# Kernel optimization log

Measured on AMD Instinct MI355X. Metric: run time of the kernel, lower is better.

Reference implementation:

```python
import jax, jax.numpy as jnp
import numpy as np

B, S, D, N, H = 4, 1024, 768, 12, 64
IGNORE = -100000.0


def setup_inputs() -> dict:
    key = jax.random.key(0)
    ks = jax.random.split(key, 9)
    std = 0.02
    return {
        "normalized_resid_pre": jax.random.normal(ks[0], (B, S, D), dtype=jnp.float32),
        "W_Q": jax.random.normal(ks[1], (N, D, H), dtype=jnp.float32) * std,
        "W_K": jax.random.normal(ks[2], (N, D, H), dtype=jnp.float32) * std,
        "W_V": jax.random.normal(ks[3], (N, D, H), dtype=jnp.float32) * std,
        "W_O": jax.random.normal(ks[4], (N, H, D), dtype=jnp.float32) * std,
        "b_Q": jnp.zeros((N, H), dtype=jnp.float32),
        "b_K": jnp.zeros((N, H), dtype=jnp.float32),
        "b_V": jnp.zeros((N, H), dtype=jnp.float32),
        "b_O": jnp.zeros((D,), dtype=jnp.float32),
    }


def reference(normalized_resid_pre, W_Q, W_K, W_V, W_O, b_Q, b_K, b_V, b_O):
    x = normalized_resid_pre  # [b, s, d]
    d_head = W_Q.shape[-1]
    # per-head projections: [b, n, s, h]
    Q = jnp.einsum("bsd,ndh->bnsh", x, W_Q) + b_Q[None, :, None, :]
    K = jnp.einsum("bsd,ndh->bnsh", x, W_K) + b_K[None, :, None, :]
    V = jnp.einsum("bsd,ndh->bnsh", x, W_V) + b_V[None, :, None, :]
    # scores [b, n, s_q, s_k]
    scores = jnp.einsum("bnqh,bnkh->bnqk", Q, K) / jnp.sqrt(jnp.float32(d_head))
    s = scores.shape[-1]
    # original: tril(scores) + triu(IGNORE, k=1) == where(causal, scores, IGNORE)
    causal = jnp.tril(jnp.ones((s, s), dtype=bool))
    masked = jnp.where(causal[None, None], scores, jnp.float32(IGNORE))
    probs = jax.nn.softmax(masked, axis=-1)
    # z [b, s_q, n, h]
    z = jnp.einsum("bnqk,bnkh->bqnh", probs, V)
    out = jnp.einsum("bqnh,nhd->bqd", z, W_O) + b_O
    return out
```

## Files before the change

### kernel.cpp

```cpp
#include <hip/hip_runtime.h>

typedef __bf16 bf16x8 __attribute__((ext_vector_type(8)));
typedef __bf16 bf16x4 __attribute__((ext_vector_type(4)));
typedef float  f32x4  __attribute__((ext_vector_type(4)));

constexpr int B_ = 4, S_ = 1024, D_ = 768, N_ = 12, H_ = 64;
constexpr int BNSH = B_ * N_ * S_ * H_;
constexpr float SCALE2 = 0.18033688011f;

__device__ __forceinline__ f32x4 mfma16(bf16x8 a, bf16x8 b, f32x4 c) {
    return __builtin_amdgcn_mfma_f32_16x16x32_bf16(a, b, c, 0, 0, 0);
}

__device__ __forceinline__ void gload16(const __bf16* g, __bf16* l) {
    __builtin_amdgcn_global_load_lds(
        (const __attribute__((address_space(1))) unsigned int*)g,
        (__attribute__((address_space(3))) unsigned int*)l, 16, 0, 0);
}

__device__ __forceinline__ void stage128x64(const __bf16* g, int ld, __bf16* lds,
                                            int wid, int lane) {
    #pragma unroll
    for (int i = 0; i < 4; ++i) {
        int cb = (wid * 4 + i) * 64;
        int chunk = cb + lane;
        int r = chunk >> 3, p = chunk & 7;
        int q = p ^ (r & 7);
        gload16(g + (size_t)r * ld + q * 8, lds + cb * 8);
    }
}
__device__ __forceinline__ void stage64x64(const __bf16* g, int ld, __bf16* lds,
                                           int wid, int lane) {
    #pragma unroll
    for (int i = 0; i < 2; ++i) {
        int cb = (wid * 2 + i) * 64;
        int chunk = cb + lane;
        int r = chunk >> 3, p = chunk & 7;
        int q = p ^ (r & 7);
        gload16(g + (size_t)r * ld + q * 8, lds + cb * 8);
    }
}

__global__ __launch_bounds__(256) void prep_kernel(
    const float* __restrict__ x,
    const float* __restrict__ wq, const float* __restrict__ wk,
    const float* __restrict__ wv, const float* __restrict__ wo,
    __bf16* __restrict__ xb, __bf16* __restrict__ wt, __bf16* __restrict__ wot) {
    __shared__ __bf16 T[64][65];
    const int blk = blockIdx.x;
    const int tid = threadIdx.x;
    if (blk < 768) {
        int base = blk * 1024 + tid;
        #pragma unroll
        for (int i = 0; i < 4; ++i) {
            int idx = base + i * 256;
            float4 v = ((const float4*)x)[idx];
            bf16x4 o;
            o[0] = (__bf16)v.x; o[1] = (__bf16)v.y;
            o[2] = (__bf16)v.z; o[3] = (__bf16)v.w;
            ((bf16x4*)xb)[idx] = o;
        }
        return;
    }
    int rr = tid >> 4, c4 = (tid & 15) * 4;
    if (blk < 1200) {
        int t = blk - 768;
        int dt = t % 12, mh = t / 12;
        int mat = mh / 12, n = mh % 12;
        const float* in = (mat == 0 ? wq : mat == 1 ? wk : wv) + (size_t)n * 768 * 64;
        __bf16* outp = wt + (size_t)(mat * 768 + n * 64) * 768;
        int d0 = dt * 64;
        #pragma unroll
        for (int i = 0; i < 4; ++i) {
            int row = rr + 16 * i;
            float4 v = *(const float4*)&in[(size_t)(d0 + row) * 64 + c4];
            T[c4 + 0][row] = (__bf16)v.x;
            T[c4 + 1][row] = (__bf16)v.y;
            T[c4 + 2][row] = (__bf16)v.z;
            T[c4 + 3][row] = (__bf16)v.w;
        }
        __syncthreads();
        #pragma unroll
        for (int i = 0; i < 4; ++i) {
            int hrow = rr + 16 * i;
            bf16x4 o;
            o[0] = T[hrow][c4 + 0]; o[1] = T[hrow][c4 + 1];
            o[2] = T[hrow][c4 + 2]; o[3] = T[hrow][c4 + 3];
            *(bf16x4*)&outp[(size_t)hrow * 768 + d0 + c4] = o;
        }
    } else {
        int t = blk - 1200;
        int r0 = (t % 12) * 64, c0 = (t / 12) * 64;
        #pragma unroll
        for (int i = 0; i < 4; ++i) {
            int row = rr + 16 * i;
            float4 v = *(const float4*)&wo[(size_t)(r0 + row) * 768 + c0 + c4];
            T[c4 + 0][row] = (__bf16)v.x;
            T[c4 + 1][row] = (__bf16)v.y;
            T[c4 + 2][row] = (__bf16)v.z;
            T[c4 + 3][row] = (__bf16)v.w;
        }
        __syncthreads();
        #pragma unroll
        for (int i = 0; i < 4; ++i) {
            int crow = rr + 16 * i;
            bf16x4 o;
            o[0] = T[crow][c4 + 0]; o[1] = T[crow][c4 + 1];
            o[2] = T[crow][c4 + 2]; o[3] = T[crow][c4 + 3];
            *(bf16x4*)&wot[(size_t)(c0 + crow) * 768 + r0 + c4] = o;
        }
    }
}

__global__ __launch_bounds__(256) void qkv_gemm(
    const __bf16* __restrict__ xb, const __bf16* __restrict__ wtg,
    const float* __restrict__ bq, const float* __restrict__ bk,
    const float* __restrict__ bv,
    __bf16* __restrict__ Qb, __bf16* __restrict__ Kb, __bf16* __restrict__ Vtb) {
    __shared__ __bf16 As[2][128 * 64];
    __shared__ __bf16 Bs[2][64 * 64];
    const int m0 = blockIdx.x * 128;
    const int j0 = blockIdx.y * 64;
    const int tid = threadIdx.x, wid = tid >> 6, lane = tid & 63;
    const int quad = lane >> 4, lrow = lane & 15;
    const int l3 = lrow & 7;
    int koff[2];
    #pragma unroll
    for (int ks = 0; ks < 2; ++ks)
        koff[ks] = lrow * 64 + ((ks * 4 + quad) ^ l3) * 8;

    f32x4 zf = {0.f, 0.f, 0.f, 0.f};
    f32x4 acc[2][4];
    #pragma unroll
    for (int i = 0; i < 2; ++i)
        #pragma unroll
        for (int j = 0; j < 4; ++j) acc[i][j] = zf;

    stage128x64(xb + (size_t)m0 * 768, 768, As[0], wid, lane);
    stage64x64(wtg + (size_t)j0 * 768, 768, Bs[0], wid, lane);

    for (int kt = 0; kt < 12; ++kt) {
        const int buf = kt & 1;
        __syncthreads();
        if (kt < 11) {
            stage128x64(xb + (size_t)m0 * 768 + (kt + 1) * 64, 768, As[buf ^ 1], wid, lane);
            stage64x64(wtg + (size_t)j0 * 768 + (kt + 1) * 64, 768, Bs[buf ^ 1], wid, lane);
        }
        #pragma unroll
        for (int ks = 0; ks < 2; ++ks) {
            bf16x8 af[2], bfr[4];
            #pragma unroll
            for (int mi = 0; mi < 2; ++mi)
                af[mi] = *(const bf16x8*)(As[buf] + (wid * 32 + mi * 16) * 64 + koff[ks]);
            #pragma unroll
            for (int ni = 0; ni < 4; ++ni)
                bfr[ni] = *(const bf16x8*)(Bs[buf] + ni * 1024 + koff[ks]);
            #pragma unroll
            for (int mi = 0; mi < 2; ++mi)
                #pragma unroll
                for (int ni = 0; ni < 4; ++ni)
                    acc[mi][ni] = mfma16(af[mi], bfr[ni], acc[mi][ni]);
        }
    }

    const int mat = j0 / 768;
    const int n = (j0 % 768) >> 6;
    const int b = m0 >> 10;
    const int s_base = (m0 & 1023) + wid * 32;
    const float* bias = (mat == 0 ? bq : mat == 1 ? bk : bv) + n * 64;
    const float osc = (mat == 0) ? SCALE2 : 1.0f;
    float bias_v[4];
    #pragma unroll
    for (int ni = 0; ni < 4; ++ni) bias_v[ni] = bias[ni * 16 + lrow];

    if (mat == 2) {
        __bf16* vout = Vtb + (size_t)(b * N_ + n) * 64 * 1024;
        #pragma unroll
        for (int mi = 0; mi < 2; ++mi)
            #pragma unroll
            for (int ni = 0; ni < 4; ++ni) {
                int h = ni * 16 + lrow;
                int s0 = s_base + mi * 16 + quad * 4;
                bf16x4 pv;
                #pragma unroll
                for (int r = 0; r < 4; ++r)
                    pv[r] = (__bf16)(acc[mi][ni][r] + bias_v[ni]);
                *(bf16x4*)(vout + (size_t)h * 1024 + s0) = pv;
            }
    } else {
        __bf16* qk = (mat == 0 ? Qb : Kb) + (size_t)(b * N_ + n) * 1024 * 64;
        #pragma unroll
        for (int mi = 0; mi < 2; ++mi)
            #pragma unroll
            for (int r = 0; r < 4; ++r) {
                int s = s_base + mi * 16 + quad * 4 + r;
                #pragma unroll
                for (int ni = 0; ni < 4; ++ni)
                    qk[(size_t)s * 64 + ni * 16 + lrow] =
                        (__bf16)((acc[mi][ni][r] + bias_v[ni]) * osc);
            }
    }
}

__global__ __launch_bounds__(256) void attn_mfma(
    const __bf16* __restrict__ Qb, const __bf16* __restrict__ Kb,
    const __bf16* __restrict__ Vtb, __bf16* __restrict__ zb) {
    __shared__ __bf16 Ks[2][64 * 64], Vs[2][64 * 64];
    __shared__ __bf16 Pt[4][16 * 64];
    const int bid = blockIdx.x;
    const int qt = 15 - bid / 48;
    const int bn = bid % 48;
    const int b = bn / N_, n = bn % N_;
    const int tid = threadIdx.x, wid = tid >> 6, lane = tid & 63;
    const int quad = lane >> 4, lrow = lane & 15;
    const int l3 = lrow & 7;
    const __bf16* Qg = Qb + (size_t)(b * N_ + n) * S_ * H_;
    const __bf16* Kg = Kb + (size_t)(b * N_ + n) * S_ * H_;
    const __bf16* Vg = Vtb + (size_t)(b * N_ + n) * H_ * S_;
    const int q0 = qt * 64;

    int koff[2];
    #pragma unroll
    for (int ks = 0; ks < 2; ++ks)
        koff[ks] = lrow * 64 + ((ks * 4 + quad) ^ l3) * 8;
    int ptw[4], ptr_[2];
    #pragma unroll
    for (int nt = 0; nt < 4; ++nt) {
        int c16 = nt * 2 + (quad >> 1);
        ptw[nt] = lrow * 64 + (c16 ^ l3) * 8 + (quad & 1) * 4;
    }
    #pragma unroll
    for (int ks = 0; ks < 2; ++ks)
        ptr_[ks] = lrow * 64 + ((ks * 4 + quad) ^ l3) * 8;

    bf16x8 qf[2];
    #pragma unroll
    for (int ks = 0; ks < 2; ++ks)
        qf[ks] = *(const bf16x8*)&Qg[(size_t)(q0 + wid * 16 + lrow) * 64
                                     + ks * 32 + quad * 8];

    stage64x64(Kg, 64, Ks[0], wid, lane);
    stage64x64(Vg, 1024, Vs[0], wid, lane);

    f32x4 zf = {0.f, 0.f, 0.f, 0.f};
    f32x4 o[4];
    #pragma unroll
    for (int i = 0; i < 4; ++i) o[i] = zf;
    float l_r = 0.f;
    __bf16* Pw = Pt[wid];
    const int myq = wid * 16 + lrow;

    auto do_tile = [&](int buf, bool diag) {
        f32x4 sc[4];
        #pragma unroll
        for (int nt = 0; nt < 4; ++nt) sc[nt] = zf;
        __builtin_amdgcn_s_setprio(1);
        #pragma unroll
        for (int ks = 0; ks < 2; ++ks) {
            #pragma unroll
            for (int nt = 0; nt < 4; ++nt) {
                bf16x8 kfr = *(const bf16x8*)(Ks[buf] + nt * 1024 + koff[ks]);
                sc[nt] = mfma16(kfr, qf[ks], sc[nt]);
            }
        }
        __builtin_amdgcn_s_setprio(0);
        if (diag) {
            #pragma unroll
            for (int nt = 0; nt < 4; ++nt)
                #pragma unroll
                for (int r = 0; r < 4; ++r)
                    if ((nt * 16 + quad * 4 + r) > myq) sc[nt][r] = -1e30f;
        }
        float rs = 0.f;
        #pragma unroll
        for (int nt = 0; nt < 4; ++nt)
            #pragma unroll
            for (int r = 0; r < 4; ++r) {
                float p = __builtin_amdgcn_exp2f(sc[nt][r]);
                sc[nt][r] = p;
                rs += p;
            }
        l_r += rs;
        #pragma unroll
        for (int nt = 0; nt < 4; ++nt) {
            bf16x4 pk;
            #pragma unroll
            for (int r = 0; r < 4; ++r) pk[r] = (__bf16)sc[nt][r];
            *(bf16x4*)(Pw + ptw[nt]) = pk;
        }
        __builtin_amdgcn_s_setprio(1);
        #pragma unroll
        for (int ks = 0; ks < 2; ++ks) {
            bf16x8 pf = *(const bf16x8*)(Pw + ptr_[ks]);
            #pragma unroll
            for (int ht = 0; ht < 4; ++ht) {
                bf16x8 vfr = *(const bf16x8*)(Vs[buf] + ht * 1024 + koff[ks]);
                o[ht] = mfma16(vfr, pf, o[ht]);
            }
        }
        __builtin_amdgcn_s_setprio(0);
    };

    for (int kt = 0; kt < qt; ++kt) {
        __syncthreads();
        stage64x64(Kg + (size_t)(kt + 1) * 64 * 64, 64, Ks[(kt + 1) & 1], wid, lane);
        stage64x64(Vg + (kt + 1) * 64, 1024, Vs[(kt + 1) & 1], wid, lane);
        do_tile(kt & 1, false);
    }
    __syncthreads();
    do_tile(qt & 1, true);

    l_r += __shfl_xor(l_r, 16);
    l_r += __shfl_xor(l_r, 32);
    const float linv = 1.0f / l_r;
    __bf16* zout = zb + (size_t)b * S_ * 768 + (size_t)(q0 + myq) * 768 + n * 64;
    #pragma unroll
    for (int ht = 0; ht < 4; ++ht) {
        bf16x4 zo;
        #pragma unroll
        for (int r = 0; r < 4; ++r) zo[r] = (__bf16)(o[ht][r] * linv);
        *(bf16x4*)&zout[ht * 16 + quad * 4] = zo;
    }
}

__global__ __launch_bounds__(256) void out_gemm(
    const __bf16* __restrict__ zb, const __bf16* __restrict__ wot,
    const float* __restrict__ bo, float* __restrict__ out) {
    __shared__ __bf16 As[2][64 * 64];
    __shared__ __bf16 Bs[2][64 * 64];
    const int m0 = blockIdx.x * 64;
    const int j0 = blockIdx.y * 64;
    const int tid = threadIdx.x, wid = tid >> 6, lane = tid & 63;
    const int quad = lane >> 4, lrow = lane & 15;
    const int l3 = lrow & 7;
    int koff[2];
    #pragma unroll
    for (int ks = 0; ks < 2; ++ks)
        koff[ks] = lrow * 64 + ((ks * 4 + quad) ^ l3) * 8;

    f32x4 zf = {0.f, 0.f, 0.f, 0.f};
    f32x4 acc[4];
    #pragma unroll
    for (int j = 0; j < 4; ++j) acc[j] = zf;

    stage64x64(zb + (size_t)m0 * 768, 768, As[0], wid, lane);
    stage64x64(wot + (size_t)j0 * 768, 768, Bs[0], wid, lane);

    for (int kt = 0; kt < 12; ++kt) {
        const int buf = kt & 1;
        __syncthreads();
        if (kt < 11) {
            stage64x64(zb + (size_t)m0 * 768 + (kt + 1) * 64, 768, As[buf ^ 1], wid, lane);
            stage64x64(wot + (size_t)j0 * 768 + (kt + 1) * 64, 768, Bs[buf ^ 1], wid, lane);
        }
        #pragma unroll
        for (int ks = 0; ks < 2; ++ks) {
            bf16x8 af = *(const bf16x8*)(As[buf] + wid * 1024 + koff[ks]);
            #pragma unroll
            for (int ni = 0; ni < 4; ++ni) {
                bf16x8 bfr = *(const bf16x8*)(Bs[buf] + ni * 1024 + koff[ks]);
                acc[ni] = mfma16(af, bfr, acc[ni]);
            }
        }
    }

    float bias_v[4];
    #pragma unroll
    for (int ni = 0; ni < 4; ++ni) bias_v[ni] = bo[j0 + ni * 16 + lrow];
    #pragma unroll
    for (int r = 0; r < 4; ++r) {
        int m = m0 + wid * 16 + quad * 4 + r;
        #pragma unroll
        for (int ni = 0; ni < 4; ++ni)
            out[(size_t)m * 768 + j0 + ni * 16 + lrow] = acc[ni][r] + bias_v[ni];
    }
}

extern "C" void kernel_launch(void* const* d_in, const int* in_sizes, int n_in,
                              void* d_out, int out_size, void* d_ws, size_t ws_size,
                              hipStream_t stream) {
    const float* x  = (const float*)d_in[0];
    const float* wq = (const float*)d_in[1];
    const float* wk = (const float*)d_in[2];
    const float* wv = (const float*)d_in[3];
    const float* wo = (const float*)d_in[4];
    const float* bq = (const float*)d_in[5];
    const float* bk = (const float*)d_in[6];
    const float* bv = (const float*)d_in[7];
    const float* bo = (const float*)d_in[8];
    float* out = (float*)d_out;

    __bf16* p   = (__bf16*)d_ws;
    __bf16* xb  = p;  p += (size_t)4096 * 768;
    __bf16* wt  = p;  p += (size_t)2304 * 768;
    __bf16* wot = p;  p += (size_t)768 * 768;
    __bf16* Qb  = p;  p += (size_t)BNSH;
    __bf16* Kb  = p;  p += (size_t)BNSH;
    __bf16* Vtb = p;  p += (size_t)BNSH;
    __bf16* zb  = p;  p += (size_t)4096 * 768;

    prep_kernel<<<1344, 256, 0, stream>>>(x, wq, wk, wv, wo, xb, wt, wot);
    qkv_gemm<<<dim3(32, 36), 256, 0, stream>>>(xb, wt, bq, bk, bv, Qb, Kb, Vtb);
    attn_mfma<<<768, 256, 0, stream>>>(Qb, Kb, Vtb, zb);
    out_gemm<<<dim3(64, 12), 256, 0, stream>>>(zb, wot, bo, out);
}
```

Baseline: 137.3 us.

## Switch attention to 32x32x16 MFMA with register-resident P via permlane swap

Rewrites the attention kernel to use 32x32x16 bf16 MFMA with two waves of 32 query rows each (128 threads) in place of four waves of 16 rows. The softmax probabilities are packed with v_cvt_pk_bf16_f32 and rearranged into the B-operand layout with v_permlane32_swap, which removes the per-wave LDS round trip for P. The aim is fewer LDS reads and writes per FLOP and larger MFMA tiles. The trade-off is fewer waves per block, higher register pressure from the 16-wide accumulators, and each thread now issuing more staging loads.

Result: slower. 141.2 us (+2.9%).

```diff
diff --git a/kernel.cpp b/kernel.cpp
--- a/kernel.cpp
+++ b/kernel.cpp
@@ -3,6 +3,7 @@
 typedef __bf16 bf16x8 __attribute__((ext_vector_type(8)));
 typedef __bf16 bf16x4 __attribute__((ext_vector_type(4)));
 typedef float  f32x4  __attribute__((ext_vector_type(4)));
+typedef float  f32x16 __attribute__((ext_vector_type(16)));
 
 constexpr int B_ = 4, S_ = 1024, D_ = 768, N_ = 12, H_ = 64;
 constexpr int BNSH = B_ * N_ * S_ * H_;
@@ -10,6 +11,15 @@
 
 __device__ __forceinline__ f32x4 mfma16(bf16x8 a, bf16x8 b, f32x4 c) {
     return __builtin_amdgcn_mfma_f32_16x16x32_bf16(a, b, c, 0, 0, 0);
+}
+__device__ __forceinline__ f32x16 mfma32(bf16x8 a, bf16x8 b, f32x16 c) {
+    return __builtin_amdgcn_mfma_f32_32x32x16_bf16(a, b, c, 0, 0, 0);
+}
+
+__device__ __forceinline__ unsigned pkbf16(float a, float b) {
+    unsigned r;
+    asm("v_cvt_pk_bf16_f32 %0, %1, %2" : "=v"(r) : "v"(a), "v"(b));
+    return r;
 }
 
 __device__ __forceinline__ void gload16(const __bf16* g, __bf16* l) {
@@ -34,6 +44,17 @@
     #pragma unroll
     for (int i = 0; i < 2; ++i) {
         int cb = (wid * 2 + i) * 64;
+        int chunk = cb + lane;
+        int r = chunk >> 3, p = chunk & 7;
+        int q = p ^ (r & 7);
+        gload16(g + (size_t)r * ld + q * 8, lds + cb * 8);
+    }
+}
+__device__ __forceinline__ void stage64x64_w2(const __bf16* g, int ld, __bf16* lds,
+                                              int wid, int lane) {
+    #pragma unroll
+    for (int i = 0; i < 4; ++i) {
+        int cb = (wid * 4 + i) * 64;
         int chunk = cb + lane;
         int r = chunk >> 3, p = chunk & 7;
         int q = p ^ (r & 7);
@@ -202,125 +223,122 @@
     }
 }
 
-__global__ __launch_bounds__(256) void attn_mfma(
+__global__ __launch_bounds__(128) void attn_mfma(
     const __bf16* __restrict__ Qb, const __bf16* __restrict__ Kb,
     const __bf16* __restrict__ Vtb, __bf16* __restrict__ zb) {
     __shared__ __bf16 Ks[2][64 * 64], Vs[2][64 * 64];
-    __shared__ __bf16 Pt[4][16 * 64];
     const int bid = blockIdx.x;
     const int qt = 15 - bid / 48;
     const int bn = bid % 48;
     const int b = bn / N_, n = bn % N_;
     const int tid = threadIdx.x, wid = tid >> 6, lane = tid & 63;
-    const int quad = lane >> 4, lrow = lane & 15;
-    const int l3 = lrow & 7;
+    const int col = lane & 31;
+    const int hi  = lane >> 5;
+    const int c7  = col & 7;
     const __bf16* Qg = Qb + (size_t)(b * N_ + n) * S_ * H_;
     const __bf16* Kg = Kb + (size_t)(b * N_ + n) * S_ * H_;
     const __bf16* Vg = Vtb + (size_t)(b * N_ + n) * H_ * S_;
     const int q0 = qt * 64;
-
-    int koff[2];
-    #pragma unroll
-    for (int ks = 0; ks < 2; ++ks)
-        koff[ks] = lrow * 64 + ((ks * 4 + quad) ^ l3) * 8;
-    int ptw[4], ptr_[2];
-    #pragma unroll
-    for (int nt = 0; nt < 4; ++nt) {
-        int c16 = nt * 2 + (quad >> 1);
-        ptw[nt] = lrow * 64 + (c16 ^ l3) * 8 + (quad & 1) * 4;
-    }
-    #pragma unroll
-    for (int ks = 0; ks < 2; ++ks)
-        ptr_[ks] = lrow * 64 + ((ks * 4 + quad) ^ l3) * 8;
-
-    bf16x8 qf[2];
-    #pragma unroll
-    for (int ks = 0; ks < 2; ++ks)
-        qf[ks] = *(const bf16x8*)&Qg[(size_t)(q0 + wid * 16 + lrow) * 64
-                                     + ks * 32 + quad * 8];
-
-    stage64x64(Kg, 64, Ks[0], wid, lane);
-    stage64x64(Vg, 1024, Vs[0], wid, lane);
-
-    f32x4 zf = {0.f, 0.f, 0.f, 0.f};
-    f32x4 o[4];
-    #pragma unroll
-    for (int i = 0; i < 4; ++i) o[i] = zf;
+    const int qloc = wid * 32 + col;
+
+    bf16x8 qf[4];
+    #pragma unroll
+    for (int kk = 0; kk < 4; ++kk)
+        qf[kk] = *(const bf16x8*)&Qg[(size_t)(q0 + qloc) * 64 + kk * 16 + hi * 8];
+
+    int rowb[2];
+    #pragma unroll
+    for (int i = 0; i < 2; ++i) rowb[i] = (i * 32 + col) * 64;
+
+    stage64x64_w2(Kg, 64, Ks[0], wid, lane);
+    stage64x64_w2(Vg, 1024, Vs[0], wid, lane);
+
+    const f32x16 zf16 = {0.f,0.f,0.f,0.f,0.f,0.f,0.f,0.f,
+                         0.f,0.f,0.f,0.f,0.f,0.f,0.f,0.f};
+    f32x16 o[2];
+    o[0] = zf16; o[1] = zf16;
     float l_r = 0.f;
-    __bf16* Pw = Pt[wid];
-    const int myq = wid * 16 + lrow;
 
     auto do_tile = [&](int buf, bool diag) {
-        f32x4 sc[4];
-        #pragma unroll
-        for (int nt = 0; nt < 4; ++nt) sc[nt] = zf;
+        f32x16 sc[2];
+        sc[0] = zf16; sc[1] = zf16;
         __builtin_amdgcn_s_setprio(1);
         #pragma unroll
-        for (int ks = 0; ks < 2; ++ks) {
-            #pragma unroll
-            for (int nt = 0; nt < 4; ++nt) {
-                bf16x8 kfr = *(const bf16x8*)(Ks[buf] + nt * 1024 + koff[ks]);
-                sc[nt] = mfma16(kfr, qf[ks], sc[nt]);
-            }
-        }
+        for (int sb = 0; sb < 2; ++sb)
+            #pragma unroll
+            for (int kk = 0; kk < 4; ++kk) {
+                bf16x8 kf = *(const bf16x8*)(Ks[buf] + rowb[sb]
+                                             + ((kk * 2 + hi) ^ c7) * 8);
+                sc[sb] = mfma32(kf, qf[kk], sc[sb]);
+            }
         __builtin_amdgcn_s_setprio(0);
         if (diag) {
             #pragma unroll
-            for (int nt = 0; nt < 4; ++nt)
+            for (int sb = 0; sb < 2; ++sb)
                 #pragma unroll
-                for (int r = 0; r < 4; ++r)
-                    if ((nt * 16 + quad * 4 + r) > myq) sc[nt][r] = -1e30f;
+                for (int r = 0; r < 16; ++r) {
+                    int sl = sb * 32 + (r & 3) + 8 * (r >> 2) + 4 * hi;
+                    if (sl > qloc) sc[sb][r] = -1e30f;
+                }
         }
         float rs = 0.f;
         #pragma unroll
-        for (int nt = 0; nt < 4; ++nt)
-            #pragma unroll
-            for (int r = 0; r < 4; ++r) {
-                float p = __builtin_amdgcn_exp2f(sc[nt][r]);
-                sc[nt][r] = p;
+        for (int sb = 0; sb < 2; ++sb)
+            #pragma unroll
+            for (int r = 0; r < 16; ++r) {
+                float p = __builtin_amdgcn_exp2f(sc[sb][r]);
+                sc[sb][r] = p;
                 rs += p;
             }
         l_r += rs;
-        #pragma unroll
-        for (int nt = 0; nt < 4; ++nt) {
-            bf16x4 pk;
-            #pragma unroll
-            for (int r = 0; r < 4; ++r) pk[r] = (__bf16)sc[nt][r];
-            *(bf16x4*)(Pw + ptw[nt]) = pk;
+        bf16x8 pf[4];
+        #pragma unroll
+        for (int kk = 0; kk < 4; ++kk) {
+            const int sb = kk >> 1, base = (kk & 1) * 8;
+            unsigned A0 = pkbf16(sc[sb][base + 0], sc[sb][base + 1]);
+            unsigned A1 = pkbf16(sc[sb][base + 2], sc[sb][base + 3]);
+            unsigned B0 = pkbf16(sc[sb][base + 4], sc[sb][base + 5]);
+            unsigned B1 = pkbf16(sc[sb][base + 6], sc[sb][base + 7]);
+            asm volatile("v_permlane32_swap_b32 %0, %1" : "+v"(A0), "+v"(B0));
+            asm volatile("v_permlane32_swap_b32 %0, %1" : "+v"(A1), "+v"(B1));
+            union { unsigned w[4]; bf16x8 v; } u;
+            u.w[0] = A0; u.w[1] = A1; u.w[2] = B0; u.w[3] = B1;
+            pf[kk] = u.v;
         }
         __builtin_amdgcn_s_setprio(1);
         #pragma unroll
-        for (int ks = 0; ks < 2; ++ks) {
-            bf16x8 pf = *(const bf16x8*)(Pw + ptr_[ks]);
-            #pragma unroll
-            for (int ht = 0; ht < 4; ++ht) {
-                bf16x8 vfr = *(const bf16x8*)(Vs[buf] + ht * 1024 + koff[ks]);
-                o[ht] = mfma16(vfr, pf, o[ht]);
-            }
-        }
+        for (int hb = 0; hb < 2; ++hb)
+            #pragma unroll
+            for (int kk = 0; kk < 4; ++kk) {
+                bf16x8 vf = *(const bf16x8*)(Vs[buf] + rowb[hb]
+                                             + ((kk * 2 + hi) ^ c7) * 8);
+                o[hb] = mfma32(vf, pf[kk], o[hb]);
+            }
         __builtin_amdgcn_s_setprio(0);
     };
 
     for (int kt = 0; kt < qt; ++kt) {
         __syncthreads();
-        stage64x64(Kg + (size_t)(kt + 1) * 64 * 64, 64, Ks[(kt + 1) & 1], wid, lane);
-        stage64x64(Vg + (kt + 1) * 64, 1024, Vs[(kt + 1) & 1], wid, lane);
+        stage64x64_w2(Kg + (size_t)(kt + 1) * 64 * 64, 64, Ks[(kt + 1) & 1], wid, lane);
+        stage64x64_w2(Vg + (kt + 1) * 64, 1024, Vs[(kt + 1) & 1], wid, lane);
         do_tile(kt & 1, false);
     }
     __syncthreads();
     do_tile(qt & 1, true);
 
-    l_r += __shfl_xor(l_r, 16);
-    l_r += __shfl_xor(l_r, 32);
-    const float linv = 1.0f / l_r;
-    __bf16* zout = zb + (size_t)b * S_ * 768 + (size_t)(q0 + myq) * 768 + n * 64;
-    #pragma unroll
-    for (int ht = 0; ht < 4; ++ht) {
-        bf16x4 zo;
-        #pragma unroll
-        for (int r = 0; r < 4; ++r) zo[r] = (__bf16)(o[ht][r] * linv);
-        *(bf16x4*)&zout[ht * 16 + quad * 4] = zo;
-    }
+    float lt = l_r + __shfl_xor(l_r, 32);
+    const float linv = 1.0f / lt;
+    __bf16* zout = zb + (size_t)b * S_ * 768 + (size_t)(q0 + qloc) * 768 + n * 64;
+    #pragma unroll
+    for (int hb = 0; hb < 2; ++hb)
+        #pragma unroll
+        for (int rq = 0; rq < 4; ++rq) {
+            bf16x4 zo;
+            #pragma unroll
+            for (int j = 0; j < 4; ++j)
+                zo[j] = (__bf16)(o[hb][rq * 4 + j] * linv);
+            *(bf16x4*)&zout[hb * 32 + rq * 8 + hi * 4] = zo;
+        }
 }
 
 __global__ __launch_bounds__(256) void out_gemm(
@@ -401,6 +419,6 @@
 
     prep_kernel<<<1344, 256, 0, stream>>>(x, wq, wk, wv, wo, xb, wt, wot);
     qkv_gemm<<<dim3(32, 36), 256, 0, stream>>>(xb, wt, bq, bk, bv, Qb, Kb, Vtb);
-    attn_mfma<<<768, 256, 0, stream>>>(Qb, Kb, Vtb, zb);
+    attn_mfma<<<768, 128, 0, stream>>>(Qb, Kb, Vtb, zb);
     out_gemm<<<dim3(64, 12), 256, 0, stream>>>(zb, wot, bo, out);
 }
```
